# Optimization experiments

Hardware: AMD Instinct MI355X
Metric: run time of the kernel (lower is better)

Reference implementation:

```python
import jax, jax.numpy as jnp
import numpy as np

B, T, D = 2, 2048, 1024
H = 16
DH = D // H
EPS = 1e-6


def setup_inputs() -> dict:
    key = jax.random.key(0)
    ks = jax.random.split(key, 9)
    s = 0.02
    return {
        "x": jax.random.normal(ks[0], (B, T, D), dtype=jnp.float32),
        "Wq": jax.random.normal(ks[1], (D, D), dtype=jnp.float32) * s,
        "bq": jnp.zeros((D,), dtype=jnp.float32),
        "Wk": jax.random.normal(ks[2], (D, D), dtype=jnp.float32) * s,
        "bk": jnp.zeros((D,), dtype=jnp.float32),
        "Wv": jax.random.normal(ks[3], (D, D), dtype=jnp.float32) * s,
        "bv": jnp.zeros((D,), dtype=jnp.float32),
        "Wo": jax.random.normal(ks[4], (D, D), dtype=jnp.float32) * s,
        "bo": jnp.zeros((D,), dtype=jnp.float32),
    }


def _feature_map(x):
    # ELU(x) + 1, the positive feature map for linear attention
    return jax.nn.elu(x) + 1.0


def reference(x, Wq, bq, Wk, bk, Wv, bv, Wo, bo):
    b, t, d = x.shape
    # projections -> (b, h, t, dh)
    q = (x @ Wq.T + bq).reshape(b, t, H, DH).transpose(0, 2, 1, 3)
    k = (x @ Wk.T + bk).reshape(b, t, H, DH).transpose(0, 2, 1, 3)
    v = (x @ Wv.T + bv).reshape(b, t, H, DH).transpose(0, 2, 1, 3)

    q = _feature_map(q)
    k = _feature_map(k)

    # causal linear attention: cumulative sums of k v^T and k over time
    kv = jnp.einsum('bhtd,bhte->bhtde', k, v)        # (b,h,t,dh,dh)
    kv_cum = jnp.cumsum(kv, axis=2)
    numerator = jnp.einsum('bhtd,bhtde->bhte', q, kv_cum)
    k_cum = jnp.cumsum(k, axis=2)
    denominator = jnp.einsum('bhtd,bhtd->bht', q, k_cum)
    denominator = jnp.maximum(denominator, EPS)[..., None]

    out = numerator / denominator                    # (b,h,t,dh)
    out = out.transpose(0, 2, 1, 3).reshape(b, t, d)
    return out @ Wo.T + bo
```

## Files before the change

kernel.cpp:

```cpp
#include <hip/hip_runtime.h>
#include <math.h>

#define BB 2
#define TT 2048
#define DD 1024
#define HH 16
#define DH 64
#define BT (BB*TT)
#define CC 64
#define NC (TT/CC)
#define EPSV 1e-6f
#define QS 3072

typedef __attribute__((ext_vector_type(8))) short short8;
typedef __attribute__((ext_vector_type(4))) float f32x4;

__device__ inline ushort f2bf(float f) {
    unsigned u = __float_as_uint(f);
    u = (u + 0x7fffu + ((u >> 16) & 1u)) >> 16;
    return (ushort)u;
}
__device__ inline float bf2f(ushort u) {
    return __uint_as_float(((unsigned)u) << 16);
}

__device__ inline void async16(const void* g, void* l) {
    __builtin_amdgcn_global_load_lds(
        (const __attribute__((address_space(1))) void*)g,
        (__attribute__((address_space(3))) void*)l, 16, 0, 0);
}

__global__ __launch_bounds__(256) void convert_pack(
    const float* __restrict__ x, const float* __restrict__ Wq,
    const float* __restrict__ Wk, const float* __restrict__ Wv,
    const float* __restrict__ Wo, const float* __restrict__ bq,
    const float* __restrict__ bk, const float* __restrict__ bv,
    ushort* __restrict__ xb, ushort* __restrict__ Wqkvb,
    ushort* __restrict__ Wob, float* __restrict__ biasq)
{
    int i = blockIdx.x * 256 + threadIdx.x;
    int idx = i * 8;
    const float* src;
    ushort* dst;
    if (idx < 4194304) { src = x + idx; dst = xb + idx; }
    else if (idx < 7340032) {
        int r = idx - 4194304;
        int w = r >> 20;
        int o = r & 1048575;
        src = (w == 0 ? Wq : (w == 1 ? Wk : Wv)) + o;
        dst = Wqkvb + r;
    } else {
        int r = idx - 7340032;
        src = Wo + r; dst = Wob + r;
    }
    float4 f0 = *(const float4*)src;
    float4 f1 = *(const float4*)(src + 4);
    *(ushort4*)dst = make_ushort4(f2bf(f0.x), f2bf(f0.y), f2bf(f0.z), f2bf(f0.w));
    *(ushort4*)(dst + 4) = make_ushort4(f2bf(f1.x), f2bf(f1.y), f2bf(f1.z), f2bf(f1.w));
    if (i < 3072)
        biasq[i] = (i < 1024) ? bq[i] : (i < 2048) ? bk[i - 1024] : bv[i - 2048];
}

#define BM 128
#define BN 128
#define BK 32

template<bool OBF16>
__global__ __launch_bounds__(256) void gemm_mfma(
    const ushort* __restrict__ A, const ushort* __restrict__ W,
    const float* __restrict__ bias, void* __restrict__ Cv,
    int M, int N, int K, int act_limit)
{
    constexpr int SMEM_US = OBF16 ? (128 * 132) : (BM * BK + BN * BK);
    __shared__ __align__(16) ushort smem[SMEM_US];
    ushort* As = smem;
    ushort* Bs = smem + BM * BK;
    int tid = threadIdx.x;
    int lane = tid & 63, wave = tid >> 6;
    int m0 = blockIdx.y * BM, n0 = blockIdx.x * BN;
    int wm = (wave >> 1) * 64, wn = (wave & 1) * 64;

    int p = lane & 3;
    int r0 = (wave * 2 + 0) * 16 + (lane >> 2);
    int r1 = (wave * 2 + 1) * 16 + (lane >> 2);
    int kg0 = p ^ ((r0 >> 1) & 3);
    int kg1 = p ^ ((r1 >> 1) & 3);
    const ushort* gA0 = A + (size_t)(m0 + r0) * K + kg0 * 8;
    const ushort* gA1 = A + (size_t)(m0 + r1) * K + kg1 * 8;
    const ushort* gB0 = W + (size_t)(n0 + r0) * K + kg0 * 8;
    const ushort* gB1 = W + (size_t)(n0 + r1) * K + kg1 * 8;
    ushort* lA0 = &As[r0 * BK + p * 8];
    ushort* lA1 = &As[r1 * BK + p * 8];
    ushort* lB0 = &Bs[r0 * BK + p * 8];
    ushort* lB1 = &Bs[r1 * BK + p * 8];

    int fr = lane & 15;
    int g = lane >> 4;
    int pk = (g ^ ((fr >> 1) & 3)) * 8;
    const ushort* aBase = &As[(wm + fr) * BK + pk];
    const ushort* bBase = &Bs[(wn + fr) * BK + pk];

    f32x4 acc[4][4];
#pragma unroll
    for (int i = 0; i < 4; i++)
#pragma unroll
        for (int j = 0; j < 4; j++) acc[i][j] = (f32x4){0.f, 0.f, 0.f, 0.f};

    for (int kt = 0; kt < K; kt += BK) {
        async16(gA0 + kt, lA0);
        async16(gA1 + kt, lA1);
        async16(gB0 + kt, lB0);
        async16(gB1 + kt, lB1);
        __syncthreads();
        short8 af[4], bf[4];
#pragma unroll
        for (int i = 0; i < 4; i++) af[i] = *(const short8*)(aBase + i * 16 * BK);
#pragma unroll
        for (int j = 0; j < 4; j++) bf[j] = *(const short8*)(bBase + j * 16 * BK);
#pragma unroll
        for (int i = 0; i < 4; i++)
#pragma unroll
            for (int j = 0; j < 4; j++)
                acc[i][j] = __builtin_amdgcn_mfma_f32_16x16x32_bf16(
                    af[i], bf[j], acc[i][j], 0, 0, 0);
        __syncthreads();
    }

    if (OBF16) {
        ushort* Cs = smem;
#pragma unroll
        for (int j = 0; j < 4; j++) {
            int colL = wn + j * 16 + fr;
            float bv_ = bias[n0 + colL];
            bool act = (n0 + colL) < act_limit;
#pragma unroll
            for (int i = 0; i < 4; i++) {
                int rowL = wm + i * 16 + g * 4;
#pragma unroll
                for (int r = 0; r < 4; r++) {
                    float v = acc[i][j][r] + bv_;
                    if (act) v = (v > 0.f) ? (v + 1.f) : expf(v);
                    Cs[(rowL + r) * 132 + colL] = f2bf(v);
                }
            }
        }
        __syncthreads();
        ushort* C = (ushort*)Cv;
        int orow = tid >> 4, ocol = (tid & 15) * 8;
#pragma unroll
        for (int it = 0; it < 8; it++) {
            int rr = orow + it * 16;
            ushort4 lo = *(const ushort4*)&Cs[rr * 132 + ocol];
            ushort4 hi = *(const ushort4*)&Cs[rr * 132 + ocol + 4];
            ushort pk8[8] = {lo.x, lo.y, lo.z, lo.w, hi.x, hi.y, hi.z, hi.w};
            *(uint4*)&C[(size_t)(m0 + rr) * N + n0 + ocol] = *(uint4*)pk8;
        }
    } else {
        float* C = (float*)Cv;
#pragma unroll
        for (int j = 0; j < 4; j++) {
            int col = n0 + wn + j * 16 + fr;
            float bv_ = bias[col];
            bool act = col < act_limit;
#pragma unroll
            for (int i = 0; i < 4; i++) {
                int rowb = m0 + wm + i * 16 + g * 4;
#pragma unroll
                for (int r = 0; r < 4; r++) {
                    float v = acc[i][j][r] + bv_;
                    if (act) v = (v > 0.f) ? (v + 1.f) : expf(v);
                    C[(size_t)(rowb + r) * N + col] = v;
                }
            }
        }
    }
}

__global__ __launch_bounds__(256) void chunk_kv_mfma(
    const ushort* __restrict__ qkv, float* __restrict__ S)
{
    __shared__ __align__(16) ushort sm[9216];
    int tid = threadIdx.x, lane = tid & 63, wave = tid >> 6;
    int blk = blockIdx.x;
    int c = blk & (NC - 1);
    int bh = blk >> 5;
    int b = bh >> 4, h = bh & 15;
    size_t rowbase = (size_t)(b * TT + c * CC) * QS + h * DH;

    int rrow = tid >> 4, rc4 = (tid & 15) * 4;
#pragma unroll
    for (int r = 0; r < 4; r++) {
        int row = rrow + r * 16;
        ushort4 k4 = *(const ushort4*)&qkv[rowbase + (size_t)row * QS + 1024 + rc4];
        ushort4 v4 = *(const ushort4*)&qkv[rowbase + (size_t)row * QS + 2048 + rc4];
#pragma unroll
        for (int j = 0; j < 4; j++) {
            int d = rc4 + j;
            int pos = (row >> 3) ^ (d & 7);
            sm[0    + d * 64 + pos * 8 + (row & 7)] = ((const ushort*)&k4)[j];
            sm[4096 + d * 64 + pos * 8 + (row & 7)] = ((const ushort*)&v4)[j];
        }
    }
    if (tid < 16) {
        ushort4 one4 = make_ushort4(0x3F80, 0x3F80, 0x3F80, 0x3F80);
        *(ushort4*)&sm[4096 + 64 * 64 + tid * 4] = one4;
    }
    __syncthreads();

    int fr = lane & 15, g = lane >> 4;
    short8 bk_[2];
#pragma unroll
    for (int kt = 0; kt < 2; kt++) {
        int row = wave * 16 + fr;
        int kg = kt * 4 + g;
        bk_[kt] = *(const short8*)&sm[0 + row * 64 + (kg ^ (row & 7)) * 8];
    }
    f32x4 acc[5];
#pragma unroll
    for (int it = 0; it < 5; it++) acc[it] = (f32x4){0.f, 0.f, 0.f, 0.f};
#pragma unroll
    for (int it = 0; it < 5; it++) {
        int arow = it * 16 + fr;
#pragma unroll
        for (int kt = 0; kt < 2; kt++) {
            int kg = kt * 4 + g;
            short8 av = *(const short8*)&sm[4096 + arow * 64 + (kg ^ (arow & 7)) * 8];
            acc[it] = __builtin_amdgcn_mfma_f32_16x16x32_bf16(av, bk_[kt], acc[it], 0, 0, 0);
        }
    }
    size_t sb = (size_t)blk * 5120;
#pragma unroll
    for (int it = 0; it < 4; it++)
#pragma unroll
        for (int r = 0; r < 4; r++) {
            int e = it * 16 + g * 4 + r;
            S[sb + e * 64 + wave * 16 + fr] = acc[it][r];
        }
    if (g == 0) S[sb + 64 * 64 + wave * 16 + fr] = acc[4][0];
}

__global__ __launch_bounds__(256) void prefix_scan(
    const float* __restrict__ S, ushort* __restrict__ SpT)
{
    int bh = blockIdx.x / 20;
    int seg = blockIdx.x % 20;
    int idx = seg * 256 + threadIdx.x;
    int e = idx >> 6, d = idx & 63;
    size_t base = (size_t)bh * NC * 5120;
    int pos = (d >> 3) ^ (e & 7);
    size_t woff = (size_t)e * 64 + pos * 8 + (d & 7);
    if (e <= 64) {
        float run = 0.f;
        for (int c = 0; c < NC; c++) {
            size_t boff = base + (size_t)c * 5120;
            float t = S[boff + idx];
            SpT[boff + woff] = f2bf(run);
            run += t;
        }
    } else {
        for (int c = 0; c < NC; c++)
            SpT[base + (size_t)c * 5120 + woff] = 0;
    }
}

__global__ __launch_bounds__(256) void attn_mfma(
    const ushort* __restrict__ qkv, const ushort* __restrict__ SpT,
    ushort* __restrict__ ob)
{
    __shared__ __align__(16) ushort sm[18432];
    const int LQ = 0, LK = 4096, LSP = 8192, LVT = 13312;
    int tid = threadIdx.x, lane = tid & 63, wave = tid >> 6;
    int blk = blockIdx.x;
    int c = blk & (NC - 1);
    int bh = blk >> 5;
    int b = bh >> 4, h = bh & 15;
    size_t rowbase = (size_t)(b * TT + c * CC) * QS + h * DH;

#pragma unroll
    for (int r = 0; r < 2; r++) {
        int slot = (r * 4 + wave) * 64 + lane;
        int row = slot >> 3, p = slot & 7;
        int kg = p ^ (row & 7);
        const ushort* gq = qkv + rowbase + (size_t)row * QS + kg * 8;
        async16(gq, &sm[LQ + slot * 8]);
        async16(gq + 1024, &sm[LK + slot * 8]);
    }
    {
        size_t spbase = (size_t)blk * 5120;
        int slot = wave * 64 + lane;
        async16(SpT + spbase + slot * 8, &sm[LSP + slot * 8]);
        async16(SpT + spbase + (slot + 256) * 8, &sm[LSP + (slot + 256) * 8]);
        if (wave < 2) {
            int s2 = 512 + wave * 64 + lane;
            async16(SpT + spbase + s2 * 8, &sm[LSP + s2 * 8]);
        }
    }
    {
        int rrow = tid >> 4, rc4 = (tid & 15) * 4;
#pragma unroll
        for (int r = 0; r < 4; r++) {
            int row = rrow + r * 16;
            ushort4 v4 = *(const ushort4*)&qkv[rowbase + (size_t)row * QS + 2048 + rc4];
#pragma unroll
            for (int j = 0; j < 4; j++) {
                int e = rc4 + j;
                int pos = (row >> 3) ^ (e & 7);
                sm[LVT + e * 64 + pos * 8 + (row & 7)] = ((const ushort*)&v4)[j];
            }
        }
        if (tid < 16) {
            ushort4 one4 = make_ushort4(0x3F80, 0x3F80, 0x3F80, 0x3F80);
            *(ushort4*)&sm[LVT + 64 * 64 + tid * 4] = one4;
        }
    }
    __syncthreads();

    int fr = lane & 15, g = lane >> 4;
    int mrow = wave * 16 + fr;

    short8 aq[2];
#pragma unroll
    for (int kt = 0; kt < 2; kt++) {
        int kg = kt * 4 + g;
        aq[kt] = *(const short8*)&sm[LQ + mrow * 64 + (kg ^ (mrow & 7)) * 8];
    }

    f32x4 accA[4];
#pragma unroll
    for (int jt = 0; jt < 4; jt++) accA[jt] = (f32x4){0.f, 0.f, 0.f, 0.f};
#pragma unroll
    for (int jt = 0; jt < 4; jt++) {
        int nrow = jt * 16 + fr;
#pragma unroll
        for (int kt = 0; kt < 2; kt++) {
            int kg = kt * 4 + g;
            short8 bk_ = *(const short8*)&sm[LK + nrow * 64 + (kg ^ (nrow & 7)) * 8];
            accA[jt] = __builtin_amdgcn_mfma_f32_16x16x32_bf16(aq[kt], bk_, accA[jt], 0, 0, 0);
        }
    }
    __syncthreads();

#pragma unroll
    for (int jt = 0; jt < 4; jt++) {
        int s = jt * 16 + fr;
#pragma unroll
        for (int r = 0; r < 4; r++) {
            int t = wave * 16 + g * 4 + r;
            float pv = (s <= t) ? accA[jt][r] : 0.f;
            int pos = (s >> 3) ^ (t & 7);
            sm[LK + t * 64 + pos * 8 + (s & 7)] = f2bf(pv);
        }
    }

    f32x4 acc[5];
#pragma unroll
    for (int jt = 0; jt < 5; jt++) acc[jt] = (f32x4){0.f, 0.f, 0.f, 0.f};
#pragma unroll
    for (int jt = 0; jt < 5; jt++) {
        int nrow = jt * 16 + fr;
#pragma unroll
        for (int kt = 0; kt < 2; kt++) {
            int kg = kt * 4 + g;
            short8 bsp = *(const short8*)&sm[LSP + nrow * 64 + (kg ^ (nrow & 7)) * 8];
            acc[jt] = __builtin_amdgcn_mfma_f32_16x16x32_bf16(aq[kt], bsp, acc[jt], 0, 0, 0);
        }
    }
    __syncthreads();

    short8 ap[2];
#pragma unroll
    for (int kt = 0; kt < 2; kt++) {
        int kg = kt * 4 + g;
        ap[kt] = *(const short8*)&sm[LK + mrow * 64 + (kg ^ (mrow & 7)) * 8];
    }
#pragma unroll
    for (int jt = 0; jt < 5; jt++) {
        int nrow = jt * 16 + fr;
#pragma unroll
        for (int kt = 0; kt < 2; kt++) {
            int kg = kt * 4 + g;
            short8 bvt = *(const short8*)&sm[LVT + nrow * 64 + (kg ^ (nrow & 7)) * 8];
            acc[jt] = __builtin_amdgcn_mfma_f32_16x16x32_bf16(ap[kt], bvt, acc[jt], 0, 0, 0);
        }
    }

    int srcl = g * 16;
    float rdi[4];
#pragma unroll
    for (int r = 0; r < 4; r++) {
        float den = __shfl(acc[4][r], srcl, 64);
        rdi[r] = 1.f / fmaxf(den, EPSV);
    }
#pragma unroll
    for (int jt = 0; jt < 4; jt++) {
        int e = jt * 16 + fr;
#pragma unroll
        for (int r = 0; r < 4; r++) {
            int t = wave * 16 + g * 4 + r;
            sm[LSP + t * 72 + e] = f2bf(acc[jt][r] * rdi[r]);
        }
    }
    __syncthreads();

#pragma unroll
    for (int it = 0; it < 2; it++) {
        int slot = it * 256 + tid;
        int row = slot >> 3, ch = slot & 7;
        ushort4 lo = *(const ushort4*)&sm[LSP + row * 72 + ch * 8];
        ushort4 hi = *(const ushort4*)&sm[LSP + row * 72 + ch * 8 + 4];
        ushort pk8[8] = {lo.x, lo.y, lo.z, lo.w, hi.x, hi.y, hi.z, hi.w};
        *(uint4*)&ob[(size_t)(b * TT + c * CC + row) * DD + h * DH + ch * 8] = *(uint4*)pk8;
    }
}

extern "C" void kernel_launch(void* const* d_in, const int* in_sizes, int n_in,
                              void* d_out, int out_size, void* d_ws, size_t ws_size,
                              hipStream_t stream) {
    const float* x  = (const float*)d_in[0];
    const float* Wq = (const float*)d_in[1];
    const float* bq = (const float*)d_in[2];
    const float* Wk = (const float*)d_in[3];
    const float* bk = (const float*)d_in[4];
    const float* Wv = (const float*)d_in[5];
    const float* bv = (const float*)d_in[6];
    const float* Wo = (const float*)d_in[7];
    const float* bo = (const float*)d_in[8];
    float* out = (float*)d_out;

    char* ws = (char*)d_ws;
    ushort* xb    = (ushort*)(ws + 0);
    ushort* Wqkvb = (ushort*)(ws + 8388608);
    ushort* Wob   = (ushort*)(ws + 14680064);
    float*  biasq = (float*)(ws + 16777216);
    ushort* qkvb  = (ushort*)(ws + 16789504);
    float*  S     = (float*)(ws + 41955328);
    ushort* SpTb  = (ushort*)(ws + 62926848);
    ushort* attnb = (ushort*)(ws + 0);

    convert_pack<<<4096, 256, 0, stream>>>(x, Wq, Wk, Wv, Wo, bq, bk, bv,
                                           xb, Wqkvb, Wob, biasq);
    gemm_mfma<true><<<dim3(3072 / BN, BT / BM), 256, 0, stream>>>(
        xb, Wqkvb, biasq, qkvb, BT, 3072, DD, 2048);
    chunk_kv_mfma<<<BB * HH * NC, 256, 0, stream>>>(qkvb, S);
    prefix_scan<<<BB * HH * 20, 256, 0, stream>>>(S, SpTb);
    attn_mfma<<<BB * HH * NC, 256, 0, stream>>>(qkvb, SpTb, attnb);
    gemm_mfma<false><<<dim3(DD / BN, BT / BM), 256, 0, stream>>>(
        attnb, Wob, bo, out, BT, DD, DD, 0);
}
```

Before: 182.6 us.

## Template GEMM tile sizes with BK=64, smaller out-proj tiles, bf16 chunk states

```diff
diff --git a/kernel.cpp b/kernel.cpp
--- a/kernel.cpp
+++ b/kernel.cpp
@@ -61,80 +61,89 @@
         biasq[i] = (i < 1024) ? bq[i] : (i < 2048) ? bk[i - 1024] : bv[i - 2048];
 }
 
-#define BM 128
-#define BN 128
-#define BK 32
-
-template<bool OBF16>
+template<int TBM, int TBN, bool OBF16>
 __global__ __launch_bounds__(256) void gemm_mfma(
     const ushort* __restrict__ A, const ushort* __restrict__ W,
     const float* __restrict__ bias, void* __restrict__ Cv,
     int M, int N, int K, int act_limit)
 {
-    constexpr int SMEM_US = OBF16 ? (128 * 132) : (BM * BK + BN * BK);
+    constexpr int IT = TBM / 32, JT = TBN / 32;
+    constexpr int APT = TBM * 8 / 256;
+    constexpr int BPT = TBN * 8 / 256;
+    constexpr int STAGE_US = (TBM + TBN) * 64;
+    constexpr int SMEM_US = (OBF16 && TBM * 132 > STAGE_US) ? TBM * 132 : STAGE_US;
     __shared__ __align__(16) ushort smem[SMEM_US];
     ushort* As = smem;
-    ushort* Bs = smem + BM * BK;
+    ushort* Bs = smem + TBM * 64;
     int tid = threadIdx.x;
     int lane = tid & 63, wave = tid >> 6;
-    int m0 = blockIdx.y * BM, n0 = blockIdx.x * BN;
-    int wm = (wave >> 1) * 64, wn = (wave & 1) * 64;
-
-    int p = lane & 3;
-    int r0 = (wave * 2 + 0) * 16 + (lane >> 2);
-    int r1 = (wave * 2 + 1) * 16 + (lane >> 2);
-    int kg0 = p ^ ((r0 >> 1) & 3);
-    int kg1 = p ^ ((r1 >> 1) & 3);
-    const ushort* gA0 = A + (size_t)(m0 + r0) * K + kg0 * 8;
-    const ushort* gA1 = A + (size_t)(m0 + r1) * K + kg1 * 8;
-    const ushort* gB0 = W + (size_t)(n0 + r0) * K + kg0 * 8;
-    const ushort* gB1 = W + (size_t)(n0 + r1) * K + kg1 * 8;
-    ushort* lA0 = &As[r0 * BK + p * 8];
-    ushort* lA1 = &As[r1 * BK + p * 8];
-    ushort* lB0 = &Bs[r0 * BK + p * 8];
-    ushort* lB1 = &Bs[r1 * BK + p * 8];
-
-    int fr = lane & 15;
-    int g = lane >> 4;
-    int pk = (g ^ ((fr >> 1) & 3)) * 8;
-    const ushort* aBase = &As[(wm + fr) * BK + pk];
-    const ushort* bBase = &Bs[(wn + fr) * BK + pk];
-
-    f32x4 acc[4][4];
-#pragma unroll
-    for (int i = 0; i < 4; i++)
-#pragma unroll
-        for (int j = 0; j < 4; j++) acc[i][j] = (f32x4){0.f, 0.f, 0.f, 0.f};
-
-    for (int kt = 0; kt < K; kt += BK) {
-        async16(gA0 + kt, lA0);
-        async16(gA1 + kt, lA1);
-        async16(gB0 + kt, lB0);
-        async16(gB1 + kt, lB1);
+    int m0 = blockIdx.y * TBM, n0 = blockIdx.x * TBN;
+    int wm = (wave >> 1) * (TBM / 2), wn = (wave & 1) * (TBN / 2);
+
+    const ushort* gA[APT]; ushort* lA[APT];
+    const ushort* gB[BPT]; ushort* lB[BPT];
+#pragma unroll
+    for (int s = 0; s < APT; s++) {
+        int slot = s * 256 + tid;
+        int row = slot >> 3, p = slot & 7, kg = p ^ (row & 7);
+        gA[s] = A + (size_t)(m0 + row) * K + kg * 8;
+        lA[s] = &As[slot * 8];
+    }
+#pragma unroll
+    for (int s = 0; s < BPT; s++) {
+        int slot = s * 256 + tid;
+        int row = slot >> 3, p = slot & 7, kg = p ^ (row & 7);
+        gB[s] = W + (size_t)(n0 + row) * K + kg * 8;
+        lB[s] = &Bs[slot * 8];
+    }
+
+    int fr = lane & 15, g = lane >> 4;
+
+    f32x4 acc[IT][JT];
+#pragma unroll
+    for (int i = 0; i < IT; i++)
+#pragma unroll
+        for (int j = 0; j < JT; j++) acc[i][j] = (f32x4){0.f, 0.f, 0.f, 0.f};
+
+    for (int kt = 0; kt < K; kt += 64) {
+#pragma unroll
+        for (int s = 0; s < APT; s++) async16(gA[s] + kt, lA[s]);
+#pragma unroll
+        for (int s = 0; s < BPT; s++) async16(gB[s] + kt, lB[s]);
         __syncthreads();
-        short8 af[4], bf[4];
-#pragma unroll
-        for (int i = 0; i < 4; i++) af[i] = *(const short8*)(aBase + i * 16 * BK);
-#pragma unroll
-        for (int j = 0; j < 4; j++) bf[j] = *(const short8*)(bBase + j * 16 * BK);
-#pragma unroll
-        for (int i = 0; i < 4; i++)
-#pragma unroll
-            for (int j = 0; j < 4; j++)
-                acc[i][j] = __builtin_amdgcn_mfma_f32_16x16x32_bf16(
-                    af[i], bf[j], acc[i][j], 0, 0, 0);
+#pragma unroll
+        for (int ks = 0; ks < 2; ks++) {
+            int kg = ks * 4 + g;
+            short8 af[IT], bf[JT];
+#pragma unroll
+            for (int i = 0; i < IT; i++) {
+                int mr = wm + i * 16 + fr;
+                af[i] = *(const short8*)&As[mr * 64 + (kg ^ (mr & 7)) * 8];
+            }
+#pragma unroll
+            for (int j = 0; j < JT; j++) {
+                int nr = wn + j * 16 + fr;
+                bf[j] = *(const short8*)&Bs[nr * 64 + (kg ^ (nr & 7)) * 8];
+            }
+#pragma unroll
+            for (int i = 0; i < IT; i++)
+#pragma unroll
+                for (int j = 0; j < JT; j++)
+                    acc[i][j] = __builtin_amdgcn_mfma_f32_16x16x32_bf16(
+                        af[i], bf[j], acc[i][j], 0, 0, 0);
+        }
         __syncthreads();
     }
 
     if (OBF16) {
         ushort* Cs = smem;
 #pragma unroll
-        for (int j = 0; j < 4; j++) {
+        for (int j = 0; j < JT; j++) {
             int colL = wn + j * 16 + fr;
             float bv_ = bias[n0 + colL];
             bool act = (n0 + colL) < act_limit;
 #pragma unroll
-            for (int i = 0; i < 4; i++) {
+            for (int i = 0; i < IT; i++) {
                 int rowL = wm + i * 16 + g * 4;
 #pragma unroll
                 for (int r = 0; r < 4; r++) {
@@ -148,7 +157,7 @@
         ushort* C = (ushort*)Cv;
         int orow = tid >> 4, ocol = (tid & 15) * 8;
 #pragma unroll
-        for (int it = 0; it < 8; it++) {
+        for (int it = 0; it < TBM / 16; it++) {
             int rr = orow + it * 16;
             ushort4 lo = *(const ushort4*)&Cs[rr * 132 + ocol];
             ushort4 hi = *(const ushort4*)&Cs[rr * 132 + ocol + 4];
@@ -158,12 +167,12 @@
     } else {
         float* C = (float*)Cv;
 #pragma unroll
-        for (int j = 0; j < 4; j++) {
+        for (int j = 0; j < JT; j++) {
             int col = n0 + wn + j * 16 + fr;
             float bv_ = bias[col];
             bool act = col < act_limit;
 #pragma unroll
-            for (int i = 0; i < 4; i++) {
+            for (int i = 0; i < IT; i++) {
                 int rowb = m0 + wm + i * 16 + g * 4;
 #pragma unroll
                 for (int r = 0; r < 4; r++) {
@@ -177,7 +186,7 @@
 }
 
 __global__ __launch_bounds__(256) void chunk_kv_mfma(
-    const ushort* __restrict__ qkv, float* __restrict__ S)
+    const ushort* __restrict__ qkv, ushort* __restrict__ S)
 {
     __shared__ __align__(16) ushort sm[9216];
     int tid = threadIdx.x, lane = tid & 63, wave = tid >> 6;
@@ -234,13 +243,13 @@
 #pragma unroll
         for (int r = 0; r < 4; r++) {
             int e = it * 16 + g * 4 + r;
-            S[sb + e * 64 + wave * 16 + fr] = acc[it][r];
-        }
-    if (g == 0) S[sb + 64 * 64 + wave * 16 + fr] = acc[4][0];
+            S[sb + e * 64 + wave * 16 + fr] = f2bf(acc[it][r]);
+        }
+    if (g == 0) S[sb + 64 * 64 + wave * 16 + fr] = f2bf(acc[4][0]);
 }
 
 __global__ __launch_bounds__(256) void prefix_scan(
-    const float* __restrict__ S, ushort* __restrict__ SpT)
+    const ushort* __restrict__ S, ushort* __restrict__ SpT)
 {
     int bh = blockIdx.x / 20;
     int seg = blockIdx.x % 20;
@@ -253,7 +262,7 @@
         float run = 0.f;
         for (int c = 0; c < NC; c++) {
             size_t boff = base + (size_t)c * 5120;
-            float t = S[boff + idx];
+            float t = bf2f(S[boff + idx]);
             SpT[boff + woff] = f2bf(run);
             run += t;
         }
@@ -433,17 +442,17 @@
     ushort* Wob   = (ushort*)(ws + 14680064);
     float*  biasq = (float*)(ws + 16777216);
     ushort* qkvb  = (ushort*)(ws + 16789504);
-    float*  S     = (float*)(ws + 41955328);
-    ushort* SpTb  = (ushort*)(ws + 62926848);
+    ushort* Sb    = (ushort*)(ws + 41955328);
+    ushort* SpTb  = (ushort*)(ws + 52441088);
     ushort* attnb = (ushort*)(ws + 0);
 
     convert_pack<<<4096, 256, 0, stream>>>(x, Wq, Wk, Wv, Wo, bq, bk, bv,
                                            xb, Wqkvb, Wob, biasq);
-    gemm_mfma<true><<<dim3(3072 / BN, BT / BM), 256, 0, stream>>>(
+    gemm_mfma<128, 128, true><<<dim3(3072 / 128, BT / 128), 256, 0, stream>>>(
         xb, Wqkvb, biasq, qkvb, BT, 3072, DD, 2048);
-    chunk_kv_mfma<<<BB * HH * NC, 256, 0, stream>>>(qkvb, S);
-    prefix_scan<<<BB * HH * 20, 256, 0, stream>>>(S, SpTb);
+    chunk_kv_mfma<<<BB * HH * NC, 256, 0, stream>>>(qkvb, Sb);
+    prefix_scan<<<BB * HH * 20, 256, 0, stream>>>(Sb, SpTb);
     attn_mfma<<<BB * HH * NC, 256, 0, stream>>>(qkvb, SpTb, attnb);
-    gemm_mfma<false><<<dim3(DD / BN, BT / BM), 256, 0, stream>>>(
+    gemm_mfma<64, 128, false><<<dim3(DD / 128, BT / 64), 256, 0, stream>>>(
         attnb, Wob, bo, out, BT, DD, DD, 0);
 }
```

New measurement: 165.9 us. -9.2%, faster.
